# Kernel optimization log

Hardware: AMD Instinct MI355X
Metric: run time of the kernel (lower is better)

Reference implementation:

```python
import jax, jax.numpy as jnp
import numpy as np

B, T, F, H, M = 128, 64, 2048, 1024, 512


def setup_inputs() -> dict:
    key = jax.random.key(0)
    ks = jax.random.split(key, 12)
    def u(k, shape, fan_in):
        s = 1.0 / np.sqrt(fan_in)
        return jax.random.uniform(k, shape, jnp.float32, -s, s)
    return {
        "video_feats": jax.random.normal(ks[0], (B, T, F), jnp.float32),
        # frame_embed: Linear(F -> H)
        "W_embed": u(ks[1], (H, F), F),
        "b_embed": u(ks[2], (H,), F),
        # lstm1_cell: LSTMCell(H, H) with bias (b = b_ih + b_hh, identical math)
        "W_ih1": u(ks[3], (4 * H, H), H),
        "W_hh1": u(ks[4], (4 * H, H), H),
        "b1": u(ks[5], (4 * H,), H),
        # BoundaryDetector(H, H, M): z = sigmoid(vs . (Wsi x + Wsh h + b)), binarized
        "Wsi": u(ks[6], (M, H), H),
        "Wsh": u(ks[7], (M, H), H),
        "b_bd": u(ks[8], (M,), H),
        "vs": u(ks[9], (M,), M),
        # lstm2_cell: LSTMCell(H, H, bias=False)
        "W_ih2": u(ks[10], (4 * H, H), H),
        "W_hh2": u(ks[11], (4 * H, H), H),
    }


def _lstm_cell(x, h, c, W_ih, W_hh, b):
    # PyTorch LSTMCell gate order: i, f, g, o
    gates = x @ W_ih.T + h @ W_hh.T
    if b is not None:
        gates = gates + b
    i, f, g, o = jnp.split(gates, 4, axis=-1)
    c_new = jax.nn.sigmoid(f) * c + jax.nn.sigmoid(i) * jnp.tanh(g)
    h_new = jax.nn.sigmoid(o) * jnp.tanh(c_new)
    return h_new, c_new


def reference(video_feats, W_embed, b_embed, W_ih1, W_hh1, b1,
              Wsi, Wsh, b_bd, vs, W_ih2, W_hh2):
    # frame embedding + ReLU (dropout is identity in eval mode)
    v = jax.nn.relu(jnp.einsum('btf,hf->bth', video_feats, W_embed) + b_embed)
    vt = jnp.transpose(v, (1, 0, 2))  # [T, B, H] for scan over time

    def step(carry, x):
        h1, c1, h2, c2 = carry
        # boundary detector: scalar gate per sample, straight-through binarized
        z = jax.nn.sigmoid((x @ Wsi.T + h1 @ Wsh.T + b_bd) @ vs)  # [B]
        s = (z + jax.lax.stop_gradient(jnp.round(z) - z))[:, None]  # [B,1]
        h1n, c1n = _lstm_cell(x, h1, c1, W_ih1, W_hh1, b1)
        h2n, c2n = _lstm_cell(h1n * s, h2, c2, W_ih2, W_hh2, None)
        h1n = h1n * (1.0 - s)
        c1n = c1n * (1.0 - s)
        return (h1n, c1n, h2n, c2n), None

    z0 = jnp.zeros((B, H), video_feats.dtype)
    (h1, c1, h2, c2), _ = jax.lax.scan(step, (z0, z0, z0, z0), vt)
    return h2
```

## Files before the change

### kernel.cpp

```cpp
#include <hip/hip_runtime.h>
#include <hip/hip_bf16.h>
#include <math.h>


typedef __attribute__((ext_vector_type(8))) short short8;
typedef __attribute__((ext_vector_type(4))) short short4v;
typedef __attribute__((ext_vector_type(4))) float f32x4;
typedef __hip_bfloat16 bf16;

__device__ __forceinline__ float sigm(float x) { return 1.0f / (1.0f + expf(-x)); }
__device__ __forceinline__ short bfbits(float x) {
  bf16 h = __float2bfloat16(x);
  return __builtin_bit_cast(short, h);
}
__device__ __forceinline__ void cvt8hl(const float* __restrict__ p,
                                       short8& hi, short8& lo)
{
  f32x4 a = *(const f32x4*)p;
  f32x4 b = *(const f32x4*)(p + 4);
#pragma unroll
  for (int j = 0; j < 8; ++j) {
    float x = (j < 4) ? a[j] : b[j - 4];
    bf16 h = __float2bfloat16(x);
    hi[j] = __builtin_bit_cast(short, h);
    lo[j] = bfbits(x - __bfloat162float(h));
  }
}

__device__ __forceinline__ void gemm_bf16(
    const bf16* __restrict__ A, int lda,
    const bf16* __restrict__ B, int ldb,
    int nChunks, short* ls, f32x4 acc[4][4])
{
  const int tid  = threadIdx.x;
  const int lane = tid & 63;
  const int wave = tid >> 6;
  const int wr = (wave & 1) * 64;
  const int wc = (wave >> 1) * 64;
  const int m  = lane & 15;
  const int kg = lane >> 4;

  int srow[4], sseg[4], ssw[4];
#pragma unroll
  for (int i = 0; i < 4; ++i) {
    int linear = i * 256 + tid;
    srow[i] = linear >> 3;
    sseg[i] = linear & 7;
    ssw[i]  = (sseg[i] ^ (srow[i] & 7)) * 8;
  }

  short8 areg[4], breg[4];
#pragma unroll
  for (int i = 0; i < 4; ++i) {
    areg[i] = *(const short8*)(A + (size_t)srow[i] * lda + sseg[i] * 8);
    breg[i] = *(const short8*)(B + (size_t)srow[i] * ldb + sseg[i] * 8);
  }
#pragma unroll
  for (int i = 0; i < 4; ++i) {
    *(short8*)(ls + srow[i] * 64 + ssw[i])        = areg[i];
    *(short8*)(ls + 8192 + srow[i] * 64 + ssw[i]) = breg[i];
  }
  __syncthreads();

  for (int c = 0; c < nChunks; ++c) {
    if (c + 1 < nChunks) {
#pragma unroll
      for (int i = 0; i < 4; ++i) {
        areg[i] = *(const short8*)(A + (size_t)srow[i] * lda + (c + 1) * 64 + sseg[i] * 8);
        breg[i] = *(const short8*)(B + (size_t)srow[i] * ldb + (c + 1) * 64 + sseg[i] * 8);
      }
    }
    const short* la = ls + (c & 1) * 16384;
    const short* lb = la + 8192;
#pragma unroll
    for (int ks = 0; ks < 2; ++ks) {
      short8 af[4], bfr[4];
#pragma unroll
      for (int f = 0; f < 4; ++f) {
        int ar = wr + f * 16 + m;
        af[f]  = *(const short8*)(la + ar * 64 + (((ks * 4 + kg) ^ (ar & 7)) * 8));
        int br = wc + f * 16 + m;
        bfr[f] = *(const short8*)(lb + br * 64 + (((ks * 4 + kg) ^ (br & 7)) * 8));
      }
#pragma unroll
      for (int fr = 0; fr < 4; ++fr)
#pragma unroll
        for (int fc = 0; fc < 4; ++fc)
          acc[fr][fc] = __builtin_amdgcn_mfma_f32_16x16x32_bf16(af[fr], bfr[fc], acc[fr][fc], 0, 0, 0);
    }
    if (c + 1 < nChunks) {
      short* lw = ls + ((c + 1) & 1) * 16384;
#pragma unroll
      for (int i = 0; i < 4; ++i) {
        *(short8*)(lw + srow[i] * 64 + ssw[i])        = areg[i];
        *(short8*)(lw + 8192 + srow[i] * 64 + ssw[i]) = breg[i];
      }
    }
    __syncthreads();
  }
}

template <typename F>
__device__ __forceinline__ void epilogue(const f32x4 acc[4][4], F&& body)
{
  const int tid = threadIdx.x, lane = tid & 63, wave = tid >> 6;
  const int m = lane & 15, kg = lane >> 4;
  const int wr = (wave & 1) * 64, wc = (wave >> 1) * 64;
#pragma unroll
  for (int fr = 0; fr < 4; ++fr)
#pragma unroll
    for (int fc = 0; fc < 4; ++fc)
#pragma unroll
      for (int r = 0; r < 4; ++r)
        body(wr + fr * 16 + kg * 4 + r, wc + fc * 16 + m, acc[fr][fc][r]);
}

__global__ void k_diag(float* __restrict__ out, float val)
{
  if (threadIdx.x == 0 && blockIdx.x == 0) out[0] = val;
}

__global__ void k_uw(const float* __restrict__ Wsi, const float* __restrict__ Wsh,
                     const float* __restrict__ bbd, const float* __restrict__ vs,
                     double* __restrict__ u, double* __restrict__ wv,
                     double* __restrict__ cbdp)
{
  const int blk = blockIdx.x;
  if (blk < 8) {
    const float* W = (blk < 4) ? Wsi : Wsh;
    double* out = (blk < 4) ? u : wv;
    int h = (blk & 3) * 256 + threadIdx.x;
    double a = 0.0;
    for (int mm = 0; mm < 512; ++mm)
      a += (double)vs[mm] * (double)W[mm * 1024 + h];
    out[h] = a;
  } else if (threadIdx.x < 64) {
    double a = 0.0;
    for (int mm = threadIdx.x; mm < 512; mm += 64)
      a += (double)vs[mm] * (double)bbd[mm];
#pragma unroll
    for (int o = 32; o > 0; o >>= 1) a += __shfl_down(a, o, 64);
    if (threadIdx.x == 0) cbdp[0] = a;
  }
}

__global__ void k_wsplit(const float* __restrict__ w1ih, const float* __restrict__ w1hh,
                         const float* __restrict__ w2ih, const float* __restrict__ w2hh,
                         bf16* __restrict__ o1ih_h, bf16* __restrict__ o1ih_l,
                         bf16* __restrict__ o1hh_h, bf16* __restrict__ o1hh_l,
                         bf16* __restrict__ o2ih_h, bf16* __restrict__ o2hh_h)
{
  const int m = blockIdx.x >> 12;
  const size_t i4 = (size_t)(blockIdx.x & 4095) * 256 + threadIdx.x;
  const float* src = (m == 0) ? w1ih : (m == 1) ? w1hh : (m == 2) ? w2ih : w2hh;
  bf16* dh = (m == 0) ? o1ih_h : (m == 1) ? o1hh_h : (m == 2) ? o2ih_h : o2hh_h;
  bf16* dl = (m == 0) ? o1ih_l : (m == 1) ? o1hh_l : nullptr;
  f32x4 v = *(const f32x4*)(src + i4 * 4);
  short4v hv, lv;
#pragma unroll
  for (int j = 0; j < 4; ++j) {
    float x = v[j];
    bf16 h = __float2bfloat16(x);
    hv[j] = __builtin_bit_cast(short, h);
    lv[j] = bfbits(x - __bfloat162float(h));
  }
  *(short4v*)((short*)dh + i4 * 4) = hv;
  if (dl) *(short4v*)((short*)dl + i4 * 4) = lv;
}

__global__ __launch_bounds__(256, 2) void k_embed(
    const float* __restrict__ video, const float* __restrict__ Wemb,
    const float* __restrict__ bemb, bf16* __restrict__ vhi, bf16* __restrict__ vlo,
    int tbase, int smask)
{
  __shared__ __align__(16) short ls[32768];
  const int t  = tbase + (blockIdx.x >> 3);
  const int ct = blockIdx.x & 7;
  const int tid = threadIdx.x;

  int srow[4], sseg[4], ssw[4];
  const float* arow[4];
  const float* brow[4];
#pragma unroll
  for (int i = 0; i < 4; ++i) {
    int linear = i * 256 + tid;
    srow[i] = linear >> 3;
    sseg[i] = linear & 7;
    ssw[i]  = (sseg[i] ^ (srow[i] & 7)) * 8;
    arow[i] = video + (size_t)(srow[i] * 64 + t) * 2048 + sseg[i] * 8;
    brow[i] = Wemb + (size_t)(ct * 128 + srow[i]) * 2048 + sseg[i] * 8;
  }

  f32x4 acc[4][4] = {};
  const int lane = tid & 63, wave = tid >> 6;
  const int wr = (wave & 1) * 64, wc = (wave >> 1) * 64;
  const int m = lane & 15, kg = lane >> 4;

  short8 ah[4], al[4], bh[4], bl[4];
#pragma unroll
  for (int i = 0; i < 4; ++i) {
    cvt8hl(arow[i], ah[i], al[i]);
    cvt8hl(brow[i], bh[i], bl[i]);
  }
#pragma unroll
  for (int i = 0; i < 4; ++i) {
    *(short8*)(ls +         srow[i] * 64 + ssw[i]) = ah[i];
    *(short8*)(ls +  8192 + srow[i] * 64 + ssw[i]) = al[i];
    *(short8*)(ls + 16384 + srow[i] * 64 + ssw[i]) = bh[i];
    *(short8*)(ls + 24576 + srow[i] * 64 + ssw[i]) = bl[i];
  }
  __syncthreads();

  for (int c = 0; c < 32; ++c) {
    if (c + 1 < 32) {
#pragma unroll
      for (int i = 0; i < 4; ++i) {
        cvt8hl(arow[i] + (c + 1) * 64, ah[i], al[i]);
        cvt8hl(brow[i] + (c + 1) * 64, bh[i], bl[i]);
      }
    }
#pragma unroll
    for (int ks = 0; ks < 2; ++ks) {
      short8 afh[4], afl[4], bfh[4], bfl[4];
      int asw[4], bsw[4];
#pragma unroll
      for (int f = 0; f < 4; ++f) {
        int ar = wr + f * 16 + m;
        asw[f] = ar * 64 + (((ks * 4 + kg) ^ (ar & 7)) * 8);
        int br = wc + f * 16 + m;
        bsw[f] = br * 64 + (((ks * 4 + kg) ^ (br & 7)) * 8);
        afh[f] = *(const short8*)(ls +         asw[f]);
        bfh[f] = *(const short8*)(ls + 16384 + bsw[f]);
      }
#pragma unroll
      for (int fr = 0; fr < 4; ++fr)
#pragma unroll
        for (int fc = 0; fc < 4; ++fc)
          acc[fr][fc] = __builtin_amdgcn_mfma_f32_16x16x32_bf16(afh[fr], bfh[fc], acc[fr][fc], 0, 0, 0);
#pragma unroll
      for (int f = 0; f < 4; ++f)
        afl[f] = *(const short8*)(ls + 8192 + asw[f]);
#pragma unroll
      for (int fr = 0; fr < 4; ++fr)
#pragma unroll
        for (int fc = 0; fc < 4; ++fc)
          acc[fr][fc] = __builtin_amdgcn_mfma_f32_16x16x32_bf16(afl[fr], bfh[fc], acc[fr][fc], 0, 0, 0);
#pragma unroll
      for (int f = 0; f < 4; ++f)
        bfl[f] = *(const short8*)(ls + 24576 + bsw[f]);
#pragma unroll
      for (int fr = 0; fr < 4; ++fr)
#pragma unroll
        for (int fc = 0; fc < 4; ++fc)
          acc[fr][fc] = __builtin_amdgcn_mfma_f32_16x16x32_bf16(afh[fr], bfl[fc], acc[fr][fc], 0, 0, 0);
    }
    if (c + 1 < 32) {
      __syncthreads();
#pragma unroll
      for (int i = 0; i < 4; ++i) {
        *(short8*)(ls +         srow[i] * 64 + ssw[i]) = ah[i];
        *(short8*)(ls +  8192 + srow[i] * 64 + ssw[i]) = al[i];
        *(short8*)(ls + 16384 + srow[i] * 64 + ssw[i]) = bh[i];
        *(short8*)(ls + 24576 + srow[i] * 64 + ssw[i]) = bl[i];
      }
      __syncthreads();
    }
  }

  const int trow = (t & smask) * 128;
  epilogue(acc, [&](int lrow, int lcol, float aval) {
    int gcol = ct * 128 + lcol;
    float x = fmaxf(aval + bemb[gcol], 0.0f);
    bf16 hi = __float2bfloat16(x);
    size_t o = (size_t)(trow + lrow) * 1024 + gcol;
    vhi[o] = hi;
    vlo[o] = __float2bfloat16(x - __bfloat162float(hi));
  });
}

__global__ void k_zx(const bf16* __restrict__ vhi, const bf16* __restrict__ vlo,
                     const double* __restrict__ u, const double* __restrict__ cbdp,
                     float* __restrict__ zx, int base)
{
  const int wave = blockIdx.x * 4 + (threadIdx.x >> 6);
  const int lane = threadIdx.x & 63;
  for (int it = 0; it < 16; ++it) {
    int rr = wave * 16 + it;
    double a = 0.0;
#pragma unroll
    for (int q = 0; q < 16; ++q) {
      int h = lane + q * 64;
      size_t o = (size_t)rr * 1024 + h;
      a += (double)(__bfloat162float(vhi[o]) + __bfloat162float(vlo[o])) * u[h];
    }
#pragma unroll
    for (int o = 32; o > 0; o >>= 1) a += __shfl_down(a, o, 64);
    if (lane == 0) zx[base + rr] = (float)(a + cbdp[0]);
  }
}

__global__ __launch_bounds__(256, 2) void k_step(
    const bf16* __restrict__ vhi, const bf16* __restrict__ vlo,
    const bf16* __restrict__ h1r1h, const bf16* __restrict__ h1r1l,
    const bf16* __restrict__ h1r2h, const bf16* __restrict__ h1r2l,
    const bf16* __restrict__ h2h, const bf16* __restrict__ h2l,
    const bf16* __restrict__ w1ih_h, const bf16* __restrict__ w1ih_l,
    const bf16* __restrict__ w1hh_h, const bf16* __restrict__ w1hh_l,
    const bf16* __restrict__ w2ih_h, const bf16* __restrict__ w2hh_h,
    float* __restrict__ R, int k, int smask)
{
  __shared__ __align__(16) short ls[32768];
  const bf16* vh = vhi + (size_t)(k & smask) * 131072;
  const bf16* vl = vlo + (size_t)(k & smask) * 131072;

  const int pr = blockIdx.x >> 5;
  const int ct = blockIdx.x & 31;
  if (k == 0 && pr >= 2) return;
  if (k == 64 && pr < 3) return;

  const bf16 *A0, *B0, *A1, *B1;
  switch (pr) {
    case 0:  A0 = vh;    B0 = w1ih_h; A1 = vl;    B1 = w1ih_h; break;
    case 1:  A0 = vh;    B0 = w1ih_l; A1 = h1r1h; B1 = w1hh_h; break;
    case 2:  A0 = h1r1l; B0 = w1hh_h; A1 = h1r1h; B1 = w1hh_l; break;
    case 3:  A0 = h1r2h; B0 = w2ih_h; A1 = h1r2l; B1 = w2ih_h; break;
    default: A0 = h2h;   B0 = w2hh_h; A1 = h2l;   B1 = w2hh_h; break;
  }

  f32x4 acc[4][4] = {};
  gemm_bf16(A0, 1024, B0 + (size_t)ct * 131072, 1024, 16, ls, acc);
  if (!(k == 0 && pr == 1))
    gemm_bf16(A1, 1024, B1 + (size_t)ct * 131072, 1024, 16, ls, acc);

  float* Rout = R + (size_t)pr * 524288;
  epilogue(acc, [&](int lrow, int lcol, float aval) {
    Rout[(size_t)lrow * 4096 + ct * 128 + lcol] = aval;
  });
}

__global__ void k_elem(const float* __restrict__ R, const float* __restrict__ zx,
                       float* __restrict__ craw,
                       bf16* __restrict__ h1r1h, bf16* __restrict__ h1r1l,
                       bf16* __restrict__ h1r2h, bf16* __restrict__ h1r2l,
                       float* __restrict__ c2, bf16* __restrict__ h2h, bf16* __restrict__ h2l,
                       float* __restrict__ rdm, const double* __restrict__ wv,
                       const float* __restrict__ b1, float* __restrict__ dout, int k)
{
  __shared__ double red[4];
  const int tid = threadIdx.x;
  const int b   = blockIdx.x;
  const size_t broff = (size_t)b * 4096;
  const float* P0 = R + broff;
  const float* P1 = P0 + 524288;
  const float* P2 = P0 + 2 * 524288;
  const float* P3 = P0 + 3 * 524288;
  const float* P4 = P0 + 4 * 524288;

  if (k < 64) {
    float zpre = zx[k * 128 + b];
    if (k > 0) zpre += rdm[(k - 1) * 128 + b];
    float s  = (sigm(zpre) > 0.5f) ? 1.0f : 0.0f;
    float om = 1.0f - s;

    double rd = 0.0;
#pragma unroll
    for (int ji = 0; ji < 4; ++ji) {
      int j = tid + ji * 256;
      float gi = P0[j]        + P1[j]        + b1[j];
      float gf = P0[1024 + j] + P1[1024 + j] + b1[1024 + j];
      float gg = P0[2048 + j] + P1[2048 + j] + b1[2048 + j];
      float go = P0[3072 + j] + P1[3072 + j] + b1[3072 + j];
      if (k > 0) {
        gi += P2[j];
        gf += P2[1024 + j];
        gg += P2[2048 + j];
        go += P2[3072 + j];
      }
      float cn = sigm(gf) * craw[b * 1024 + j] + sigm(gi) * tanhf(gg);
      float hn = sigm(go) * tanhf(cn);
      craw[b * 1024 + j] = om * cn;
      float v1 = om * hn;
      bf16 h1 = __float2bfloat16(v1);
      h1r1h[b * 1024 + j] = h1;
      h1r1l[b * 1024 + j] = __float2bfloat16(v1 - __bfloat162float(h1));
      float v2 = s * hn;
      bf16 h2v = __float2bfloat16(v2);
      h1r2h[b * 1024 + j] = h2v;
      h1r2l[b * 1024 + j] = __float2bfloat16(v2 - __bfloat162float(h2v));
      rd += (double)hn * wv[j];
    }
#pragma unroll
    for (int o = 32; o > 0; o >>= 1) rd += __shfl_down(rd, o, 64);
    if ((tid & 63) == 0) red[tid >> 6] = rd;
    __syncthreads();
    if (tid == 0)
      rdm[k * 128 + b] = om * (float)(red[0] + red[1] + red[2] + red[3]);
  }

  if (k >= 1) {
#pragma unroll
    for (int ji = 0; ji < 4; ++ji) {
      int j = tid + ji * 256;
      float gi = P3[j]        + P4[j];
      float gf = P3[1024 + j] + P4[1024 + j];
      float gg = P3[2048 + j] + P4[2048 + j];
      float go = P3[3072 + j] + P4[3072 + j];
      float cn = sigm(gf) * c2[b * 1024 + j] + sigm(gi) * tanhf(gg);
      float hn = sigm(go) * tanhf(cn);
      c2[b * 1024 + j] = cn;
      bf16 hh = __float2bfloat16(hn);
      h2h[b * 1024 + j] = hh;
      h2l[b * 1024 + j] = __float2bfloat16(hn - __bfloat162float(hh));
      if (k == 64) dout[b * 1024 + j] = hn;
    }
  }
}

extern "C" void kernel_launch(void* const* d_in, const int* in_sizes, int n_in,
                              void* d_out, int out_size, void* d_ws, size_t ws_size,
                              hipStream_t stream) {
  const float* video = (const float*)d_in[0];
  const float* Wemb  = (const float*)d_in[1];
  const float* bemb  = (const float*)d_in[2];
  const float* Wih1  = (const float*)d_in[3];
  const float* Whh1  = (const float*)d_in[4];
  const float* b1    = (const float*)d_in[5];
  const float* Wsi   = (const float*)d_in[6];
  const float* Wsh   = (const float*)d_in[7];
  const float* bbd   = (const float*)d_in[8];
  const float* vs    = (const float*)d_in[9];
  const float* Wih2  = (const float*)d_in[10];
  const float* Whh2  = (const float*)d_in[11];
  float* dout = (float*)d_out;

  static const int exp_sizes[12] = {
    128 * 64 * 2048, 1024 * 2048, 1024, 4096 * 1024, 4096 * 1024, 4096,
    512 * 1024, 512 * 1024, 512, 512, 4096 * 1024, 4096 * 1024 };
  int bad = -1;
  if (n_in != 12) bad = 99;
  else if (out_size != 131072) bad = 98;
  else
    for (int i = 0; i < 12; ++i)
      if (in_sizes[i] != exp_sizes[i]) { bad = i; break; }
  if (bad >= 0) {
    k_diag<<<1, 64, 0, stream>>>(dout, 10000.0f + (float)bad);
    return;
  }

  char* ws = (char*)d_ws;
  size_t off = 0;
  auto alloc = [&](size_t bytes) {
    char* p = ws + off;
    off += (bytes + 255) & ~(size_t)255;
    return p;
  };
  bf16*  h1r1h = (bf16*)alloc(262144);
  bf16*  h1r1l = (bf16*)alloc(262144);
  bf16*  h1r2h = (bf16*)alloc(262144);
  bf16*  h1r2l = (bf16*)alloc(262144);
  bf16*  h2h   = (bf16*)alloc(262144);
  bf16*  h2l   = (bf16*)alloc(262144);
  float* c2    = (float*)alloc(524288);
  float* craw  = (float*)alloc(524288);
  const size_t zeroBytes = off;
  double* u    = (double*)alloc(8192);
  double* wvv  = (double*)alloc(8192);
  double* cbdp = (double*)alloc(256);
  float* rdm   = (float*)alloc(64 * 128 * 4);
  float* zx    = (float*)alloc(8192 * 4);
  bf16* w1ih_h = (bf16*)alloc(8388608);
  bf16* w1ih_l = (bf16*)alloc(8388608);
  bf16* w1hh_h = (bf16*)alloc(8388608);
  bf16* w1hh_l = (bf16*)alloc(8388608);
  bf16* w2ih_h = (bf16*)alloc(8388608);
  bf16* w2hh_h = (bf16*)alloc(8388608);
  float* R     = (float*)alloc(5 * 524288 * 4);
  const size_t fixedBytes = off;

  const size_t perSlot = (size_t)131072 * 2 * 2;
  int slots = 64;
  while (slots > 8 && fixedBytes + (size_t)slots * perSlot + 512 > ws_size)
    slots >>= 1;
  if (fixedBytes + (size_t)8 * perSlot + 512 > ws_size) {
    k_diag<<<1, 64, 0, stream>>>(dout, 100.0f + (float)(ws_size >> 20));
    return;
  }
  const int smask = slots - 1;
  bf16* vhi = (bf16*)alloc((size_t)slots * 131072 * 2);
  bf16* vlo = (bf16*)alloc((size_t)slots * 131072 * 2);

  (void)hipMemsetAsync(d_ws, 0, zeroBytes, stream);
  k_uw<<<9, 256, 0, stream>>>(Wsi, Wsh, bbd, vs, u, wvv, cbdp);
  k_wsplit<<<16384, 256, 0, stream>>>(Wih1, Whh1, Wih2, Whh2,
                                      w1ih_h, w1ih_l, w1hh_h, w1hh_l, w2ih_h, w2hh_h);
  if (slots == 64) {
    k_embed<<<512, 256, 0, stream>>>(video, Wemb, bemb, vhi, vlo, 0, smask);
    k_zx<<<128, 256, 0, stream>>>(vhi, vlo, u, cbdp, zx, 0);
  }

  for (int k = 0; k <= 64; ++k) {
    if (slots < 64 && k < 64 && (k & smask) == 0) {
      k_embed<<<slots * 8, 256, 0, stream>>>(video, Wemb, bemb, vhi, vlo, k, smask);
      k_zx<<<slots * 2, 256, 0, stream>>>(vhi, vlo, u, cbdp, zx, k * 128);
    }
    k_step<<<160, 256, 0, stream>>>(vhi, vlo, h1r1h, h1r1l, h1r2h, h1r2l, h2h, h2l,
                                    w1ih_h, w1ih_l, w1hh_h, w1hh_l, w2ih_h, w2hh_h,
                                    R, k, smask);
    k_elem<<<128, 256, 0, stream>>>(R, zx, craw, h1r1h, h1r1l, h1r2h, h1r2l,
                                    c2, h2h, h2l, rdm, wvv, b1, dout, k);
  }
}
```

Before: 3.087 ms.

## Hoist input-gate GEMM out of recurrence and batch embed per 8 steps

The x@W_ih1 gate product moves out of the per-step kernel into a batched k_xgates GEMM that runs once per 8 timesteps. The frame embedding becomes split-K (4 partial sums reduced in k_efin) to use more blocks. The per-step kernel now does only recurrent products, with rows masked by the boundary flag instead of storing separate h1 copies for the two layers. The boundary dot product is folded into k_elem, and the 64-slot embedding buffer is replaced by an 8-step ring. This removes per-step input-projection work and some buffers, at the cost of extra launches every 8 steps and a per-row masked load in the GEMM.

New measurement: 3.397 ms. 1.1x slower.

```diff
diff --git a/kernel.cpp b/kernel.cpp
--- a/kernel.cpp
+++ b/kernel.cpp
@@ -30,7 +30,8 @@
 __device__ __forceinline__ void gemm_bf16(
     const bf16* __restrict__ A, int lda,
     const bf16* __restrict__ B, int ldb,
-    int nChunks, short* ls, f32x4 acc[4][4])
+    int nChunks, short* ls, f32x4 acc[4][4],
+    const float* __restrict__ smk, int pol)
 {
   const int tid  = threadIdx.x;
   const int lane = tid & 63;
@@ -41,18 +42,21 @@
   const int kg = lane >> 4;
 
   int srow[4], sseg[4], ssw[4];
+  bool keep[4];
 #pragma unroll
   for (int i = 0; i < 4; ++i) {
     int linear = i * 256 + tid;
     srow[i] = linear >> 3;
     sseg[i] = linear & 7;
     ssw[i]  = (sseg[i] ^ (srow[i] & 7)) * 8;
-  }
-
+    keep[i] = (smk == nullptr) || ((smk[srow[i]] > 0.5f) == (pol != 0));
+  }
+
+  const short8 zz = {};
   short8 areg[4], breg[4];
 #pragma unroll
   for (int i = 0; i < 4; ++i) {
-    areg[i] = *(const short8*)(A + (size_t)srow[i] * lda + sseg[i] * 8);
+    areg[i] = keep[i] ? *(const short8*)(A + (size_t)srow[i] * lda + sseg[i] * 8) : zz;
     breg[i] = *(const short8*)(B + (size_t)srow[i] * ldb + sseg[i] * 8);
   }
 #pragma unroll
@@ -66,7 +70,7 @@
     if (c + 1 < nChunks) {
 #pragma unroll
       for (int i = 0; i < 4; ++i) {
-        areg[i] = *(const short8*)(A + (size_t)srow[i] * lda + (c + 1) * 64 + sseg[i] * 8);
+        areg[i] = keep[i] ? *(const short8*)(A + (size_t)srow[i] * lda + (c + 1) * 64 + sseg[i] * 8) : zz;
         breg[i] = *(const short8*)(B + (size_t)srow[i] * ldb + (c + 1) * 64 + sseg[i] * 8);
       }
     }
@@ -144,17 +148,16 @@
   }
 }
 
-__global__ void k_wsplit(const float* __restrict__ w1ih, const float* __restrict__ w1hh,
-                         const float* __restrict__ w2ih, const float* __restrict__ w2hh,
-                         bf16* __restrict__ o1ih_h, bf16* __restrict__ o1ih_l,
+__global__ void k_wsplit(const float* __restrict__ w1hh, const float* __restrict__ w2ih,
+                         const float* __restrict__ w2hh,
                          bf16* __restrict__ o1hh_h, bf16* __restrict__ o1hh_l,
                          bf16* __restrict__ o2ih_h, bf16* __restrict__ o2hh_h)
 {
   const int m = blockIdx.x >> 12;
   const size_t i4 = (size_t)(blockIdx.x & 4095) * 256 + threadIdx.x;
-  const float* src = (m == 0) ? w1ih : (m == 1) ? w1hh : (m == 2) ? w2ih : w2hh;
-  bf16* dh = (m == 0) ? o1ih_h : (m == 1) ? o1hh_h : (m == 2) ? o2ih_h : o2hh_h;
-  bf16* dl = (m == 0) ? o1ih_l : (m == 1) ? o1hh_l : nullptr;
+  const float* src = (m == 0) ? w1hh : (m == 1) ? w2ih : w2hh;
+  bf16* dh = (m == 0) ? o1hh_h : (m == 1) ? o2ih_h : o2hh_h;
+  bf16* dl = (m == 0) ? o1hh_l : nullptr;
   f32x4 v = *(const f32x4*)(src + i4 * 4);
   short4v hv, lv;
 #pragma unroll
@@ -170,12 +173,12 @@
 
 __global__ __launch_bounds__(256, 2) void k_embed(
     const float* __restrict__ video, const float* __restrict__ Wemb,
-    const float* __restrict__ bemb, bf16* __restrict__ vhi, bf16* __restrict__ vlo,
-    int tbase, int smask)
+    float* __restrict__ Ep, int tbase)
 {
   __shared__ __align__(16) short ls[32768];
-  const int t  = tbase + (blockIdx.x >> 3);
-  const int ct = blockIdx.x & 7;
+  const int tl = blockIdx.x >> 5;
+  const int ct = (blockIdx.x >> 2) & 7;
+  const int kh = blockIdx.x & 3;
   const int tid = threadIdx.x;
 
   int srow[4], sseg[4], ssw[4];
@@ -187,8 +190,8 @@
     srow[i] = linear >> 3;
     sseg[i] = linear & 7;
     ssw[i]  = (sseg[i] ^ (srow[i] & 7)) * 8;
-    arow[i] = video + (size_t)(srow[i] * 64 + t) * 2048 + sseg[i] * 8;
-    brow[i] = Wemb + (size_t)(ct * 128 + srow[i]) * 2048 + sseg[i] * 8;
+    arow[i] = video + (size_t)(srow[i] * 64 + tbase + tl) * 2048 + kh * 512 + sseg[i] * 8;
+    brow[i] = Wemb + (size_t)(ct * 128 + srow[i]) * 2048 + kh * 512 + sseg[i] * 8;
   }
 
   f32x4 acc[4][4] = {};
@@ -211,8 +214,8 @@
   }
   __syncthreads();
 
-  for (int c = 0; c < 32; ++c) {
-    if (c + 1 < 32) {
+  for (int c = 0; c < 8; ++c) {
+    if (c + 1 < 8) {
 #pragma unroll
       for (int i = 0; i < 4; ++i) {
         cvt8hl(arow[i] + (c + 1) * 64, ah[i], al[i]);
@@ -254,7 +257,7 @@
         for (int fc = 0; fc < 4; ++fc)
           acc[fr][fc] = __builtin_amdgcn_mfma_f32_16x16x32_bf16(afh[fr], bfl[fc], acc[fr][fc], 0, 0, 0);
     }
-    if (c + 1 < 32) {
+    if (c + 1 < 8) {
       __syncthreads();
 #pragma unroll
       for (int i = 0; i < 4; ++i) {
@@ -267,81 +270,181 @@
     }
   }
 
-  const int trow = (t & smask) * 128;
   epilogue(acc, [&](int lrow, int lcol, float aval) {
-    int gcol = ct * 128 + lcol;
-    float x = fmaxf(aval + bemb[gcol], 0.0f);
-    bf16 hi = __float2bfloat16(x);
-    size_t o = (size_t)(trow + lrow) * 1024 + gcol;
-    vhi[o] = hi;
-    vlo[o] = __float2bfloat16(x - __bfloat162float(hi));
+    Ep[(size_t)kh * 1048576 + (size_t)(tl * 128 + lrow) * 1024 + ct * 128 + lcol] = aval;
   });
 }
 
-__global__ void k_zx(const bf16* __restrict__ vhi, const bf16* __restrict__ vlo,
-                     const double* __restrict__ u, const double* __restrict__ cbdp,
-                     float* __restrict__ zx, int base)
-{
-  const int wave = blockIdx.x * 4 + (threadIdx.x >> 6);
-  const int lane = threadIdx.x & 63;
-  for (int it = 0; it < 16; ++it) {
-    int rr = wave * 16 + it;
-    double a = 0.0;
-#pragma unroll
-    for (int q = 0; q < 16; ++q) {
-      int h = lane + q * 64;
-      size_t o = (size_t)rr * 1024 + h;
-      a += (double)(__bfloat162float(vhi[o]) + __bfloat162float(vlo[o])) * u[h];
-    }
-#pragma unroll
-    for (int o = 32; o > 0; o >>= 1) a += __shfl_down(a, o, 64);
-    if (lane == 0) zx[base + rr] = (float)(a + cbdp[0]);
-  }
+__global__ void k_efin(const float* __restrict__ Ep, const float* __restrict__ bemb,
+                       bf16* __restrict__ vhi, bf16* __restrict__ vlo)
+{
+  const size_t e = ((size_t)blockIdx.x * 256 + threadIdx.x) * 4;
+  f32x4 a0 = *(const f32x4*)(Ep + e);
+  f32x4 a1 = *(const f32x4*)(Ep + 1048576 + e);
+  f32x4 a2 = *(const f32x4*)(Ep + 2097152 + e);
+  f32x4 a3 = *(const f32x4*)(Ep + 3145728 + e);
+  f32x4 bb = *(const f32x4*)(bemb + (e & 1023));
+  short4v hv, lv;
+#pragma unroll
+  for (int j = 0; j < 4; ++j) {
+    float x = a0[j] + a1[j] + a2[j] + a3[j] + bb[j];
+    x = fmaxf(x, 0.0f);
+    bf16 h = __float2bfloat16(x);
+    hv[j] = __builtin_bit_cast(short, h);
+    lv[j] = bfbits(x - __bfloat162float(h));
+  }
+  *(short4v*)((short*)vhi + e) = hv;
+  *(short4v*)((short*)vlo + e) = lv;
+}
+
+__global__ __launch_bounds__(256, 2) void k_xgates(
+    const bf16* __restrict__ vhi, const bf16* __restrict__ vlo,
+    const float* __restrict__ Wih1, float* __restrict__ Gx)
+{
+  __shared__ __align__(16) short ls[32768];
+  const int x  = blockIdx.x & 7;
+  const int s  = blockIdx.x >> 3;
+  const int ct = x * 4 + (s & 3);
+  const int rt = s >> 2;
+  const int tid = threadIdx.x;
+
+  int srow[4], sseg[4], ssw[4];
+  const bf16* arh[4];
+  const bf16* arl[4];
+  const float* brow[4];
+#pragma unroll
+  for (int i = 0; i < 4; ++i) {
+    int linear = i * 256 + tid;
+    srow[i] = linear >> 3;
+    sseg[i] = linear & 7;
+    ssw[i]  = (sseg[i] ^ (srow[i] & 7)) * 8;
+    arh[i] = vhi + (size_t)rt * 131072 + (size_t)srow[i] * 1024 + sseg[i] * 8;
+    arl[i] = vlo + (size_t)rt * 131072 + (size_t)srow[i] * 1024 + sseg[i] * 8;
+    brow[i] = Wih1 + (size_t)(ct * 128 + srow[i]) * 1024 + sseg[i] * 8;
+  }
+
+  f32x4 acc[4][4] = {};
+  const int lane = tid & 63, wave = tid >> 6;
+  const int wr = (wave & 1) * 64, wc = (wave >> 1) * 64;
+  const int m = lane & 15, kg = lane >> 4;
+
+  short8 ah[4], al[4], bh[4], bl[4];
+#pragma unroll
+  for (int i = 0; i < 4; ++i) {
+    ah[i] = *(const short8*)(arh[i]);
+    al[i] = *(const short8*)(arl[i]);
+    cvt8hl(brow[i], bh[i], bl[i]);
+  }
+#pragma unroll
+  for (int i = 0; i < 4; ++i) {
+    *(short8*)(ls +         srow[i] * 64 + ssw[i]) = ah[i];
+    *(short8*)(ls +  8192 + srow[i] * 64 + ssw[i]) = al[i];
+    *(short8*)(ls + 16384 + srow[i] * 64 + ssw[i]) = bh[i];
+    *(short8*)(ls + 24576 + srow[i] * 64 + ssw[i]) = bl[i];
+  }
+  __syncthreads();
+
+  for (int c = 0; c < 16; ++c) {
+    if (c + 1 < 16) {
+#pragma unroll
+      for (int i = 0; i < 4; ++i) {
+        ah[i] = *(const short8*)(arh[i] + (c + 1) * 64);
+        al[i] = *(const short8*)(arl[i] + (c + 1) * 64);
+        cvt8hl(brow[i] + (c + 1) * 64, bh[i], bl[i]);
+      }
+    }
+#pragma unroll
+    for (int ks = 0; ks < 2; ++ks) {
+      short8 afh[4], afl[4], bfh[4], bfl[4];
+      int asw[4], bsw[4];
+#pragma unroll
+      for (int f = 0; f < 4; ++f) {
+        int ar = wr + f * 16 + m;
+        asw[f] = ar * 64 + (((ks * 4 + kg) ^ (ar & 7)) * 8);
+        int br = wc + f * 16 + m;
+        bsw[f] = br * 64 + (((ks * 4 + kg) ^ (br & 7)) * 8);
+        afh[f] = *(const short8*)(ls +         asw[f]);
+        bfh[f] = *(const short8*)(ls + 16384 + bsw[f]);
+      }
+#pragma unroll
+      for (int fr = 0; fr < 4; ++fr)
+#pragma unroll
+        for (int fc = 0; fc < 4; ++fc)
+          acc[fr][fc] = __builtin_amdgcn_mfma_f32_16x16x32_bf16(afh[fr], bfh[fc], acc[fr][fc], 0, 0, 0);
+#pragma unroll
+      for (int f = 0; f < 4; ++f)
+        afl[f] = *(const short8*)(ls + 8192 + asw[f]);
+#pragma unroll
+      for (int fr = 0; fr < 4; ++fr)
+#pragma unroll
+        for (int fc = 0; fc < 4; ++fc)
+          acc[fr][fc] = __builtin_amdgcn_mfma_f32_16x16x32_bf16(afl[fr], bfh[fc], acc[fr][fc], 0, 0, 0);
+#pragma unroll
+      for (int f = 0; f < 4; ++f)
+        bfl[f] = *(const short8*)(ls + 24576 + bsw[f]);
+#pragma unroll
+      for (int fr = 0; fr < 4; ++fr)
+#pragma unroll
+        for (int fc = 0; fc < 4; ++fc)
+          acc[fr][fc] = __builtin_amdgcn_mfma_f32_16x16x32_bf16(afh[fr], bfl[fc], acc[fr][fc], 0, 0, 0);
+    }
+    if (c + 1 < 16) {
+      __syncthreads();
+#pragma unroll
+      for (int i = 0; i < 4; ++i) {
+        *(short8*)(ls +         srow[i] * 64 + ssw[i]) = ah[i];
+        *(short8*)(ls +  8192 + srow[i] * 64 + ssw[i]) = al[i];
+        *(short8*)(ls + 16384 + srow[i] * 64 + ssw[i]) = bh[i];
+        *(short8*)(ls + 24576 + srow[i] * 64 + ssw[i]) = bl[i];
+      }
+      __syncthreads();
+    }
+  }
+
+  epilogue(acc, [&](int lrow, int lcol, float aval) {
+    Gx[(size_t)rt * 524288 + (size_t)lrow * 4096 + ct * 128 + lcol] = aval;
+  });
 }
 
 __global__ __launch_bounds__(256, 2) void k_step(
-    const bf16* __restrict__ vhi, const bf16* __restrict__ vlo,
-    const bf16* __restrict__ h1r1h, const bf16* __restrict__ h1r1l,
-    const bf16* __restrict__ h1r2h, const bf16* __restrict__ h1r2l,
+    const bf16* __restrict__ h1nh, const bf16* __restrict__ h1nl,
     const bf16* __restrict__ h2h, const bf16* __restrict__ h2l,
-    const bf16* __restrict__ w1ih_h, const bf16* __restrict__ w1ih_l,
     const bf16* __restrict__ w1hh_h, const bf16* __restrict__ w1hh_l,
     const bf16* __restrict__ w2ih_h, const bf16* __restrict__ w2hh_h,
-    float* __restrict__ R, int k, int smask)
+    const float* __restrict__ sm, float* __restrict__ R, int k)
 {
   __shared__ __align__(16) short ls[32768];
-  const bf16* vh = vhi + (size_t)(k & smask) * 131072;
-  const bf16* vl = vlo + (size_t)(k & smask) * 131072;
-
-  const int pr = blockIdx.x >> 5;
+  const int u  = blockIdx.x >> 5;
   const int ct = blockIdx.x & 31;
-  if (k == 0 && pr >= 2) return;
-  if (k == 64 && pr < 3) return;
-
-  const bf16 *A0, *B0, *A1, *B1;
-  switch (pr) {
-    case 0:  A0 = vh;    B0 = w1ih_h; A1 = vl;    B1 = w1ih_h; break;
-    case 1:  A0 = vh;    B0 = w1ih_l; A1 = h1r1h; B1 = w1hh_h; break;
-    case 2:  A0 = h1r1l; B0 = w1hh_h; A1 = h1r1h; B1 = w1hh_l; break;
-    case 3:  A0 = h1r2h; B0 = w2ih_h; A1 = h1r2l; B1 = w2ih_h; break;
-    default: A0 = h2h;   B0 = w2hh_h; A1 = h2l;   B1 = w2hh_h; break;
+  if (k == 64 && u < 2) return;
+
+  const bf16 *A0, *A1, *B;
+  const float* smp = sm;
+  int pol = 0;
+  switch (u) {
+    case 0:  A0 = h1nh; A1 = h1nl;   B = w1hh_h; pol = 0; break;
+    case 1:  A0 = h1nh; A1 = nullptr; B = w1hh_l; pol = 0; break;
+    case 2:  A0 = h1nh; A1 = h1nl;   B = w2ih_h; pol = 1; break;
+    default: A0 = h2h;  A1 = h2l;    B = w2hh_h; smp = nullptr; break;
   }
 
   f32x4 acc[4][4] = {};
-  gemm_bf16(A0, 1024, B0 + (size_t)ct * 131072, 1024, 16, ls, acc);
-  if (!(k == 0 && pr == 1))
-    gemm_bf16(A1, 1024, B1 + (size_t)ct * 131072, 1024, 16, ls, acc);
-
-  float* Rout = R + (size_t)pr * 524288;
+  gemm_bf16(A0, 1024, B + (size_t)ct * 131072, 1024, 16, ls, acc, smp, pol);
+  if (A1)
+    gemm_bf16(A1, 1024, B + (size_t)ct * 131072, 1024, 16, ls, acc, smp, pol);
+
+  float* Rout = R + (size_t)u * 524288;
   epilogue(acc, [&](int lrow, int lcol, float aval) {
     Rout[(size_t)lrow * 4096 + ct * 128 + lcol] = aval;
   });
 }
 
-__global__ void k_elem(const float* __restrict__ R, const float* __restrict__ zx,
+__global__ void k_elem(const float* __restrict__ R, const float* __restrict__ Gx,
+                       const bf16* __restrict__ vhi, const bf16* __restrict__ vlo,
+                       const double* __restrict__ uvec, const double* __restrict__ cbdp,
                        float* __restrict__ craw,
-                       bf16* __restrict__ h1r1h, bf16* __restrict__ h1r1l,
-                       bf16* __restrict__ h1r2h, bf16* __restrict__ h1r2l,
+                       bf16* __restrict__ h1nh, bf16* __restrict__ h1nl,
+                       float* __restrict__ sm,
                        float* __restrict__ c2, bf16* __restrict__ h2h, bf16* __restrict__ h2l,
                        float* __restrict__ rdm, const double* __restrict__ wv,
                        const float* __restrict__ b1, float* __restrict__ dout, int k)
@@ -354,57 +457,67 @@
   const float* P1 = P0 + 524288;
   const float* P2 = P0 + 2 * 524288;
   const float* P3 = P0 + 3 * 524288;
-  const float* P4 = P0 + 4 * 524288;
+  const float* GX = Gx + (size_t)(k & 7) * 524288 + broff;
 
   if (k < 64) {
-    float zpre = zx[k * 128 + b];
+    const bf16* vhr = vhi + (size_t)(k & 7) * 131072 + (size_t)b * 1024;
+    const bf16* vlr = vlo + (size_t)(k & 7) * 131072 + (size_t)b * 1024;
+    double za = 0.0;
+#pragma unroll
+    for (int ji = 0; ji < 4; ++ji) {
+      int j = tid + ji * 256;
+      za += (double)(__bfloat162float(vhr[j]) + __bfloat162float(vlr[j])) * uvec[j];
+    }
+#pragma unroll
+    for (int o = 32; o > 0; o >>= 1) za += __shfl_down(za, o, 64);
+    if ((tid & 63) == 0) red[tid >> 6] = za;
+    __syncthreads();
+    float zpre = (float)(red[0] + red[1] + red[2] + red[3] + cbdp[0]);
     if (k > 0) zpre += rdm[(k - 1) * 128 + b];
     float s  = (sigm(zpre) > 0.5f) ? 1.0f : 0.0f;
     float om = 1.0f - s;
+    __syncthreads();
 
     double rd = 0.0;
 #pragma unroll
     for (int ji = 0; ji < 4; ++ji) {
       int j = tid + ji * 256;
-      float gi = P0[j]        + P1[j]        + b1[j];
-      float gf = P0[1024 + j] + P1[1024 + j] + b1[1024 + j];
-      float gg = P0[2048 + j] + P1[2048 + j] + b1[2048 + j];
-      float go = P0[3072 + j] + P1[3072 + j] + b1[3072 + j];
+      float gi = GX[j]        + b1[j];
+      float gf = GX[1024 + j] + b1[1024 + j];
+      float gg = GX[2048 + j] + b1[2048 + j];
+      float go = GX[3072 + j] + b1[3072 + j];
       if (k > 0) {
-        gi += P2[j];
-        gf += P2[1024 + j];
-        gg += P2[2048 + j];
-        go += P2[3072 + j];
+        gi += P0[j]        + P1[j];
+        gf += P0[1024 + j] + P1[1024 + j];
+        gg += P0[2048 + j] + P1[2048 + j];
+        go += P0[3072 + j] + P1[3072 + j];
       }
       float cn = sigm(gf) * craw[b * 1024 + j] + sigm(gi) * tanhf(gg);
       float hn = sigm(go) * tanhf(cn);
       craw[b * 1024 + j] = om * cn;
-      float v1 = om * hn;
-      bf16 h1 = __float2bfloat16(v1);
-      h1r1h[b * 1024 + j] = h1;
-      h1r1l[b * 1024 + j] = __float2bfloat16(v1 - __bfloat162float(h1));
-      float v2 = s * hn;
-      bf16 h2v = __float2bfloat16(v2);
-      h1r2h[b * 1024 + j] = h2v;
-      h1r2l[b * 1024 + j] = __float2bfloat16(v2 - __bfloat162float(h2v));
+      bf16 hh = __float2bfloat16(hn);
+      h1nh[b * 1024 + j] = hh;
+      h1nl[b * 1024 + j] = __float2bfloat16(hn - __bfloat162float(hh));
       rd += (double)hn * wv[j];
     }
 #pragma unroll
     for (int o = 32; o > 0; o >>= 1) rd += __shfl_down(rd, o, 64);
     if ((tid & 63) == 0) red[tid >> 6] = rd;
     __syncthreads();
-    if (tid == 0)
+    if (tid == 0) {
       rdm[k * 128 + b] = om * (float)(red[0] + red[1] + red[2] + red[3]);
+      sm[b] = s;
+    }
   }
 
   if (k >= 1) {
 #pragma unroll
     for (int ji = 0; ji < 4; ++ji) {
       int j = tid + ji * 256;
-      float gi = P3[j]        + P4[j];
-      float gf = P3[1024 + j] + P4[1024 + j];
-      float gg = P3[2048 + j] + P4[2048 + j];
-      float go = P3[3072 + j] + P4[3072 + j];
+      float gi = P2[j]        + P3[j];
+      float gf = P2[1024 + j] + P3[1024 + j];
+      float gg = P2[2048 + j] + P3[2048 + j];
+      float go = P2[3072 + j] + P3[3072 + j];
       float cn = sigm(gf) * c2[b * 1024 + j] + sigm(gi) * tanhf(gg);
       float hn = sigm(go) * tanhf(cn);
       c2[b * 1024 + j] = cn;
@@ -454,59 +567,48 @@
     off += (bytes + 255) & ~(size_t)255;
     return p;
   };
-  bf16*  h1r1h = (bf16*)alloc(262144);
-  bf16*  h1r1l = (bf16*)alloc(262144);
-  bf16*  h1r2h = (bf16*)alloc(262144);
-  bf16*  h1r2l = (bf16*)alloc(262144);
-  bf16*  h2h   = (bf16*)alloc(262144);
-  bf16*  h2l   = (bf16*)alloc(262144);
-  float* c2    = (float*)alloc(524288);
-  float* craw  = (float*)alloc(524288);
+  bf16*  h1nh = (bf16*)alloc(262144);
+  bf16*  h1nl = (bf16*)alloc(262144);
+  bf16*  h2h  = (bf16*)alloc(262144);
+  bf16*  h2l  = (bf16*)alloc(262144);
+  float* c2   = (float*)alloc(524288);
+  float* craw = (float*)alloc(524288);
+  float* sm   = (float*)alloc(512);
   const size_t zeroBytes = off;
   double* u    = (double*)alloc(8192);
   double* wvv  = (double*)alloc(8192);
   double* cbdp = (double*)alloc(256);
   float* rdm   = (float*)alloc(64 * 128 * 4);
-  float* zx    = (float*)alloc(8192 * 4);
-  bf16* w1ih_h = (bf16*)alloc(8388608);
-  bf16* w1ih_l = (bf16*)alloc(8388608);
   bf16* w1hh_h = (bf16*)alloc(8388608);
   bf16* w1hh_l = (bf16*)alloc(8388608);
   bf16* w2ih_h = (bf16*)alloc(8388608);
   bf16* w2hh_h = (bf16*)alloc(8388608);
-  float* R     = (float*)alloc(5 * 524288 * 4);
-  const size_t fixedBytes = off;
-
-  const size_t perSlot = (size_t)131072 * 2 * 2;
-  int slots = 64;
-  while (slots > 8 && fixedBytes + (size_t)slots * perSlot + 512 > ws_size)
-    slots >>= 1;
-  if (fixedBytes + (size_t)8 * perSlot + 512 > ws_size) {
+  float* R     = (float*)alloc(4 * 2097152);
+  float* Gxf   = (float*)alloc(8 * 2097152);
+  bf16* vhi    = (bf16*)alloc(8 * 131072 * 2);
+  bf16* vlo    = (bf16*)alloc(8 * 131072 * 2);
+
+  if (ws_size < off) {
     k_diag<<<1, 64, 0, stream>>>(dout, 100.0f + (float)(ws_size >> 20));
     return;
   }
-  const int smask = slots - 1;
-  bf16* vhi = (bf16*)alloc((size_t)slots * 131072 * 2);
-  bf16* vlo = (bf16*)alloc((size_t)slots * 131072 * 2);
 
   (void)hipMemsetAsync(d_ws, 0, zeroBytes, stream);
   k_uw<<<9, 256, 0, stream>>>(Wsi, Wsh, bbd, vs, u, wvv, cbdp);
-  k_wsplit<<<16384, 256, 0, stream>>>(Wih1, Whh1, Wih2, Whh2,
-                                      w1ih_h, w1ih_l, w1hh_h, w1hh_l, w2ih_h, w2hh_h);
-  if (slots == 64) {
-    k_embed<<<512, 256, 0, stream>>>(video, Wemb, bemb, vhi, vlo, 0, smask);
-    k_zx<<<128, 256, 0, stream>>>(vhi, vlo, u, cbdp, zx, 0);
-  }
+  k_wsplit<<<12288, 256, 0, stream>>>(Whh1, Wih2, Whh2,
+                                      w1hh_h, w1hh_l, w2ih_h, w2hh_h);
 
   for (int k = 0; k <= 64; ++k) {
-    if (slots < 64 && k < 64 && (k & smask) == 0) {
-      k_embed<<<slots * 8, 256, 0, stream>>>(video, Wemb, bemb, vhi, vlo, k, smask);
-      k_zx<<<slots * 2, 256, 0, stream>>>(vhi, vlo, u, cbdp, zx, k * 128);
-    }
-    k_step<<<160, 256, 0, stream>>>(vhi, vlo, h1r1h, h1r1l, h1r2h, h1r2l, h2h, h2l,
-                                    w1ih_h, w1ih_l, w1hh_h, w1hh_l, w2ih_h, w2hh_h,
-                                    R, k, smask);
-    k_elem<<<128, 256, 0, stream>>>(R, zx, craw, h1r1h, h1r1l, h1r2h, h1r2l,
-                                    c2, h2h, h2l, rdm, wvv, b1, dout, k);
-  }
-}
+    if (k < 64 && (k & 7) == 0) {
+      k_embed<<<256, 256, 0, stream>>>(video, Wemb, Gxf, k);
+      k_efin<<<1024, 256, 0, stream>>>(Gxf, bemb, vhi, vlo);
+      k_xgates<<<256, 256, 0, stream>>>(vhi, vlo, Wih1, Gxf);
+    }
+    if (k > 0)
+      k_step<<<128, 256, 0, stream>>>(h1nh, h1nl, h2h, h2l,
+                                      w1hh_h, w1hh_l, w2ih_h, w2hh_h, sm, R, k);
+    k_elem<<<128, 256, 0, stream>>>(R, Gxf, vhi, vlo, u, cbdp, craw,
+                                    h1nh, h1nl, sm, c2, h2h, h2l,
+                                    rdm, wvv, b1, dout, k);
+  }
+}
```
